# Kernel tuning notes

Hardware: AMD Instinct MI355X
Metric: run time of the kernel (lower is better)

The kernel has to match this reference:

```python
import jax, jax.numpy as jnp
import numpy as np

N, E, C, ED = 50000, 800000, 128, 16
NEG_SLOPE = 0.2


def setup_inputs() -> dict:
    key = jax.random.key(0)
    ks = jax.random.split(key, 18)
    inp = {
        "h": jax.random.normal(ks[0], (N, C), jnp.float32),
        "edge_index": jax.random.randint(ks[1], (2, E), 0, N),
        "edge_attr": jax.random.normal(ks[2], (E, ED), jnp.float32),
        "reducible": jax.random.randint(ks[3], (N,), 0, 2) > 0,
    }
    names = ["W", "att_src", "att_dst", "W_edge", "att_edge", "W_res", "bias"]
    shapes = [(C, C), (C,), (C,), (ED, C), (C,), (C, C), (C,)]
    i = 4
    for pre in ["red_", "irr_"]:
        for n, sh in zip(names, shapes):
            inp[pre + n] = jax.random.normal(ks[i], sh, jnp.float32) * 0.05
            i += 1
    return inp


def _gat_conv(h, src, dst, edge_attr, W, att_src, att_dst, W_edge, att_edge, W_res, bias):
    """PyG GATConv (heads=1, residual=True, add_self_loops=True, fill_value='mean')."""
    n = h.shape[0]
    # self-loop edge_attr = mean of incoming edge_attr per node (0 if none)
    sum_attr = jax.ops.segment_sum(edge_attr, dst, num_segments=n)
    cnt = jax.ops.segment_sum(jnp.ones((edge_attr.shape[0],), edge_attr.dtype), dst, num_segments=n)
    mean_attr = sum_attr / jnp.maximum(cnt, 1.0)[:, None]
    loop = jnp.arange(n)
    s = jnp.concatenate([src, loop])   # [E+N]
    d = jnp.concatenate([dst, loop])   # [E+N]
    ea = jnp.concatenate([edge_attr, mean_attr], axis=0)  # [E+N, ED]
    x = h @ W                              # [N, C]
    a_src = x @ att_src                    # [N]
    a_dst = x @ att_dst                    # [N]
    a_edge = (ea @ W_edge) @ att_edge      # [E+N]
    alpha = jax.nn.leaky_relu(a_src[s] + a_dst[d] + a_edge, NEG_SLOPE)
    # per-destination softmax (every node has a self-loop -> denom > 0)
    m = jax.ops.segment_max(alpha, d, num_segments=n)
    ex = jnp.exp(alpha - m[d])
    denom = jax.ops.segment_sum(ex, d, num_segments=n)
    w = ex / denom[d]                      # [E+N]
    out = jax.ops.segment_sum(w[:, None] * x[s], d, num_segments=n)  # [N, C]
    return out + h @ W_res + bias


def reference(h, edge_index, edge_attr, reducible,
              red_W, red_att_src, red_att_dst, red_W_edge, red_att_edge, red_W_res, red_bias,
              irr_W, irr_att_src, irr_att_dst, irr_W_edge, irr_att_edge, irr_W_res, irr_bias):
    src, dst = edge_index[0], edge_index[1]
    out_r = _gat_conv(h, src, dst, edge_attr, red_W, red_att_src, red_att_dst,
                      red_W_edge, red_att_edge, red_W_res, red_bias)
    out_i = _gat_conv(h, src, dst, edge_attr, irr_W, irr_att_src, irr_att_dst,
                      irr_W_edge, irr_att_edge, irr_W_res, irr_bias)
    return jax.nn.relu(jnp.where(reducible[:, None], out_r, out_i))
```

## Files before the change

### kernel.cpp

```cpp
#include <hip/hip_runtime.h>
#include <hip/hip_bf16.h>

#define CDIM 128
#define EDIM 16
#define NEG_SLOPE 0.2f

typedef __attribute__((ext_vector_type(8))) short bf16x8;
typedef __attribute__((ext_vector_type(4))) float f32x4;
typedef __attribute__((ext_vector_type(2))) float f32x2;
typedef unsigned int uint;
typedef unsigned short ushort;

__device__ __forceinline__ ushort f2bf(float f) {
    uint u = __float_as_uint(f);
    return (ushort)((u + 0x7fffu + ((u >> 16) & 1u)) >> 16);
}
__device__ __forceinline__ uint packbf(float lo, float hi) {
    return ((uint)f2bf(hi) << 16) | (uint)f2bf(lo);
}
__device__ __forceinline__ float bflo(uint w) { return __uint_as_float(w << 16); }
__device__ __forceinline__ float bfhi(uint w) { return __uint_as_float(w & 0xffff0000u); }

__device__ __forceinline__ bool redtest(const void* red, int i, int notInt, int notFloat) {
    if (!notInt)        return ((const int*)red)[i] != 0;
    else if (!notFloat) return ((const float*)red)[i] != 0.f;
    else                return ((const unsigned char*)red)[i] != 0;
}

__global__ void bcatwe_kernel(const float* __restrict__ Wr, const float* __restrict__ Wi,
                              const float* __restrict__ Wrr, const float* __restrict__ Wri,
                              ushort* __restrict__ BT,
                              const float* __restrict__ WeR, const float* __restrict__ aeR,
                              const float* __restrict__ WeI, const float* __restrict__ aeI,
                              float* __restrict__ we) {
    if (blockIdx.x < 256) {
        int idx = blockIdx.x * 256 + threadIdx.x;
        int c = idx >> 7, k = idx & 127;
        const float* srcm;
        if (c < 128)      srcm = Wr;
        else if (c < 256) srcm = Wi;
        else if (c < 384) srcm = Wrr;
        else              srcm = Wri;
        BT[idx] = f2bf(srcm[k * 128 + (c & 127)]);
    } else {
        int lane = threadIdx.x;
        if (lane < 16) {
            float s = 0.f;
            for (int c = 0; c < CDIM; ++c) s += WeR[lane * CDIM + c] * aeR[c];
            we[lane] = s;
        } else if (lane < 32) {
            int j = lane - 16;
            float s = 0.f;
            for (int c = 0; c < CDIM; ++c) s += WeI[j * CDIM + c] * aeI[c];
            we[16 + j] = s;
        }
    }
}

__global__ __launch_bounds__(256) void prep_kernel(const uint* __restrict__ red, int nwords,
                                                   int* __restrict__ flags,
                                                   const int* __restrict__ dst, int* __restrict__ cnt,
                                                   int* __restrict__ rank,
                                                   const float* __restrict__ ea, const float* __restrict__ we,
                                                   uint* __restrict__ escal4,
                                                   const float* __restrict__ h, ushort* __restrict__ hbf,
                                                   int E, int n4) {
    int i = blockIdx.x * 256 + threadIdx.x;
    if (i < nwords) {
        uint w = red[i];
        bool isInt = (w <= 1u);
        bool isFloat = (w == 0u) || (w == 0x3f800000u);
        if (!isInt) atomicOr(&flags[0], 1);
        if (!isFloat) atomicOr(&flags[1], 1);
    }
    if (i < E) {
        int r = atomicAdd(&cnt[dst[i]], 1);
        __builtin_nontemporal_store(r, rank + i);
        const f32x4* row = (const f32x4*)(ea + (size_t)i * EDIM);
        const float4* we4 = (const float4*)we;
        float er = 0.f, ei = 0.f;
#pragma unroll
        for (int q = 0; q < 4; ++q) {
            f32x4 v = __builtin_nontemporal_load(row + q);
            float4 wr = we4[q], wi = we4[4 + q];
            er += v.x * wr.x + v.y * wr.y + v.z * wr.z + v.w * wr.w;
            ei += v.x * wi.x + v.y * wi.y + v.z * wi.z + v.w * wi.w;
        }
        __builtin_nontemporal_store(packbf(er, ei), escal4 + i);
    }
    if (i < n4) {
        f32x4 v = __builtin_nontemporal_load((const f32x4*)h + i);
        uint2 o;
        o.x = packbf(v.x, v.y);
        o.y = packbf(v.z, v.w);
        ((uint2*)hbf)[i] = o;
    }
}

__global__ __launch_bounds__(256) void gemm_dots(const ushort* __restrict__ A,
                                                 const ushort* __restrict__ BT,
                                                 ushort* __restrict__ C,
                                                 const float* __restrict__ attsr, const float* __restrict__ attdr,
                                                 const float* __restrict__ attsi, const float* __restrict__ attdi,
                                                 float* __restrict__ asr, float* __restrict__ adr,
                                                 float* __restrict__ asi, float* __restrict__ adi,
                                                 int M) {
    __shared__ ushort As[128 * 128];
    __shared__ ushort Bs[128 * 128];
    __shared__ float dots[4][128];
    int t = threadIdx.x;
    int lane = t & 63, wv = t >> 6;
    int rb = blockIdx.x * 128;

    if (t < 128) { dots[0][t] = 0.f; dots[1][t] = 0.f; dots[2][t] = 0.f; dots[3][t] = 0.f; }

    int rsub = wv * 4 + (lane >> 4);
    int c0 = lane & 15;
#pragma unroll
    for (int p = 0; p < 8; ++p) {
        int row = p * 16 + rsub;
        int chunk = c0 ^ (row & 7);
        int gra = rb + row; if (gra > M - 1) gra = M - 1;
        const ushort* ga = A + (size_t)gra * 128 + chunk * 8;
        __builtin_amdgcn_global_load_lds(
            (const __attribute__((address_space(1))) void*)ga,
            (__attribute__((address_space(3))) void*)((char*)As + p * 4096 + wv * 1024),
            16, 0, 0);
    }

    int wr = wv >> 1, wc = wv & 1;
    int l15 = lane & 15, l4 = lane >> 4;
    const char* Ab = (const char*)As;
    const char* Bb = (const char*)Bs;

    for (int s = 0; s < 4; ++s) {
#pragma unroll
        for (int p = 0; p < 8; ++p) {
            int row = p * 16 + rsub;
            int chunk = c0 ^ (row & 7);
            const ushort* gb = BT + (size_t)(s * 128 + row) * 128 + chunk * 8;
            __builtin_amdgcn_global_load_lds(
                (const __attribute__((address_space(1))) void*)gb,
                (__attribute__((address_space(3))) void*)((char*)Bs + p * 4096 + wv * 1024),
                16, 0, 0);
        }
        __syncthreads();

        f32x4 acc[4][4];
#pragma unroll
        for (int i = 0; i < 4; ++i)
#pragma unroll
            for (int j = 0; j < 4; ++j) acc[i][j] = (f32x4){0.f, 0.f, 0.f, 0.f};

#pragma unroll
        for (int ks = 0; ks < 4; ++ks) {
            bf16x8 a[4], b[4];
#pragma unroll
            for (int f = 0; f < 4; ++f) {
                int row = wr * 64 + f * 16 + l15;
                int ch = (ks * 4 + l4) ^ (row & 7);
                a[f] = *(const bf16x8*)(Ab + row * 256 + ch * 16);
                int col = wc * 64 + f * 16 + l15;
                int ch2 = (ks * 4 + l4) ^ (col & 7);
                b[f] = *(const bf16x8*)(Bb + col * 256 + ch2 * 16);
            }
#pragma unroll
            for (int i = 0; i < 4; ++i)
#pragma unroll
                for (int j = 0; j < 4; ++j)
                    acc[i][j] = __builtin_amdgcn_mfma_f32_16x16x32_bf16(a[i], b[j], acc[i][j], 0, 0, 0);
        }

        if (s < 2) {
            const float* attS = s ? attsi : attsr;
            const float* attD = s ? attdi : attdr;
            float aS[4], aD[4];
#pragma unroll
            for (int j = 0; j < 4; ++j) {
                int c = wc * 64 + j * 16 + l15;
                aS[j] = attS[c]; aD[j] = attD[c];
            }
#pragma unroll
            for (int i = 0; i < 4; ++i)
#pragma unroll
                for (int rr = 0; rr < 4; ++rr) {
                    float ps = 0.f, pd = 0.f;
#pragma unroll
                    for (int j = 0; j < 4; ++j) {
                        float v = acc[i][j][rr];
                        ps += v * aS[j]; pd += v * aD[j];
                    }
#pragma unroll
                    for (int d = 1; d < 16; d <<= 1) {
                        ps += __shfl_xor(ps, d); pd += __shfl_xor(pd, d);
                    }
                    if (l15 == 0) {
                        int row = wr * 64 + i * 16 + l4 * 4 + rr;
                        atomicAdd(&dots[s * 2 + 0][row], ps);
                        atomicAdd(&dots[s * 2 + 1][row], pd);
                    }
                }
        }

#pragma unroll
        for (int i = 0; i < 4; ++i) {
            int rl = wr * 64 + i * 16 + l4 * 4;
#pragma unroll
            for (int j = 0; j < 4; ++j) {
                int col = s * 128 + wc * 64 + j * 16 + l15;
#pragma unroll
                for (int r = 0; r < 4; ++r) {
                    int gr = rb + rl + r;
                    if (gr < M) C[(size_t)gr * 512 + col] = f2bf(acc[i][j][r]);
                }
            }
        }
        __syncthreads();
    }

    if (t < 128) {
        int gr = rb + t;
        if (gr < M) {
            asr[gr] = dots[0][t]; adr[gr] = dots[1][t];
            asi[gr] = dots[2][t]; adi[gr] = dots[3][t];
        }
    }
}

__global__ __launch_bounds__(256) void scanA_kernel(const int* __restrict__ cnt,
                                                    int* __restrict__ offA,
                                                    int* __restrict__ bsum, int n) {
    __shared__ int wsum[4];
    int t = threadIdx.x, lane = t & 63, wid = t >> 6;
    int i0 = blockIdx.x * 1024 + t * 4;
    int v[4];
#pragma unroll
    for (int j = 0; j < 4; ++j) { int i = i0 + j; v[j] = (i < n) ? cnt[i] : 0; }
    int s = v[0] + v[1] + v[2] + v[3];
    int incl = s;
#pragma unroll
    for (int d = 1; d < 64; d <<= 1) { int u = __shfl_up(incl, d); if (lane >= d) incl += u; }
    if (lane == 63) wsum[wid] = incl;
    __syncthreads();
    int wpre = 0;
    for (int w = 0; w < wid; ++w) wpre += wsum[w];
    int run = wpre + incl - s;
#pragma unroll
    for (int j = 0; j < 4; ++j) {
        int i = i0 + j;
        if (i < n) offA[i] = run;
        run += v[j];
    }
    if (t == 255) bsum[blockIdx.x] = wpre + incl;
}

__global__ void scanB_kernel(int* __restrict__ bsum, int nb) {
    int lane = threadIdx.x;
    int carry = 0;
    for (int base = 0; base < nb; base += 64) {
        int i = base + lane;
        int v = (i < nb) ? bsum[i] : 0;
        int incl = v;
#pragma unroll
        for (int d = 1; d < 64; d <<= 1) { int u = __shfl_up(incl, d); if (lane >= d) incl += u; }
        if (i < nb) bsum[i] = carry + incl - v;
        carry += __shfl(incl, 63);
    }
}

__global__ __launch_bounds__(256) void scatter_kernel(
    const int* __restrict__ src, const int* __restrict__ dst,
    const int* __restrict__ rank, const uint* __restrict__ escal4,
    const void* __restrict__ red, const int* __restrict__ flags,
    const int* __restrict__ offA, const int* __restrict__ bsum,
    uint* __restrict__ csr, int E) {
    int e = blockIdx.x * 256 + threadIdx.x;
    if (e >= E) return;
    int s = __builtin_nontemporal_load(src + e);
    int d = __builtin_nontemporal_load(dst + e);
    uint ee = __builtin_nontemporal_load(escal4 + e);
    int rk = __builtin_nontemporal_load(rank + e);
    int notInt = flags[0], notFloat = flags[1];
    bool rr = redtest(red, d, notInt, notFloat);
    uint evb = rr ? (ee & 0xffffu) : (ee >> 16);
    int off = offA[d] + bsum[d >> 10];
    csr[off + rk] = (uint)s | (evb << 16);
}

__global__ __launch_bounds__(256) void node_kernel(
    const ushort* __restrict__ xcat,
    const float* __restrict__ adst_r, const float* __restrict__ adst_i,
    const float* __restrict__ asrc_r, const float* __restrict__ asrc_i,
    const void* __restrict__ red, const int* __restrict__ flags,
    const int* __restrict__ offA, const int* __restrict__ bsum,
    const uint* __restrict__ csr,
    const float* __restrict__ bias_r, const float* __restrict__ bias_i,
    float* __restrict__ out, int n, int E) {
    __shared__ uint2 buf[4][64];
    int wv = threadIdx.x >> 6, lane = threadIdx.x & 63;
    int node = blockIdx.x * 4 + wv;
    if (node >= n) return;

    int notInt = flags[0], notFloat = flags[1];
    bool r = redtest(red, node, notInt, notFloat);

    const float* asrc = r ? asrc_r : asrc_i;
    float adst = (r ? adst_r : adst_i)[node];
    uint vsel = r ? 0u : 256u;
    int b0 = offA[node] + bsum[node >> 10];
    int b1 = (node + 1 < n) ? (offA[node + 1] + bsum[(node + 1) >> 10]) : E;
    int k = b1 - b0;
    const char* xb = (const char*)xcat;
    uint lane4 = lane * 4;

    float m = -1e30f, denom = 0.f;
    float2 acca = make_float2(0.f, 0.f), accb = make_float2(0.f, 0.f);
    float sumE = 0.f;

    for (int base = b0; base < b1; base += 64) {
        int j = base + lane;
        float al = -1e30f; uint soff = 0;
        if (j < b1) {
            uint rec = __builtin_nontemporal_load(csr + j);
            uint s = rec & 0xffffu;
            float ev = bfhi(rec);
            sumE += ev;
            soff = s * 1024u + vsel;
            float a = asrc[s] + ev + adst;
            al = (a >= 0.f) ? a : NEG_SLOPE * a;
        }
        float cm = al;
#pragma unroll
        for (int d = 32; d; d >>= 1) cm = fmaxf(cm, __shfl_xor(cm, d));
        float mn = fmaxf(m, cm);
        float sc = __expf(m - mn);
        denom *= sc;
        acca.x *= sc; acca.y *= sc; accb.x *= sc; accb.y *= sc;
        m = mn;
        float ex = (j < b1) ? __expf(al - mn) : 0.f;
        buf[wv][lane] = make_uint2(__float_as_uint(ex), soff);
        __builtin_amdgcn_wave_barrier();
        int cc = min(64, b1 - base);
        int ccp = (cc + 7) & ~7;
        for (int tq = 0; tq < ccp; tq += 8) {
            uint2 u[8];
#pragma unroll
            for (int q = 0; q < 8; ++q) u[q] = buf[wv][tq + q];
            uint v[8];
#pragma unroll
            for (int q = 0; q < 8; ++q) v[q] = *(const uint*)(xb + u[q].y + lane4);
#pragma unroll
            for (int q = 0; q < 4; ++q) {
                float w = __uint_as_float(u[q].x);
                acca.x += w * bflo(v[q]); acca.y += w * bfhi(v[q]);
            }
#pragma unroll
            for (int q = 4; q < 8; ++q) {
                float w = __uint_as_float(u[q].x);
                accb.x += w * bflo(v[q]); accb.y += w * bfhi(v[q]);
            }
        }
        float exs = ex;
#pragma unroll
        for (int d = 32; d; d >>= 1) exs += __shfl_xor(exs, d);
        denom += exs;
        __builtin_amdgcn_wave_barrier();
    }
    float acc0 = acca.x + accb.x, acc1 = acca.y + accb.y;

#pragma unroll
    for (int d = 32; d; d >>= 1) sumE += __shfl_xor(sumE, d);
    float eself = sumE / fmaxf((float)k, 1.f);
    float a = asrc[node] + adst + eself;
    float aself = (a >= 0.f) ? a : NEG_SLOPE * a;
    float mn = fmaxf(m, aself);
    float sc = __expf(m - mn);
    float exl = __expf(aself - mn);
    denom = denom * sc + exl;
    uint voff = (uint)node * 1024u + vsel;
    uint vsw = *(const uint*)(xb + voff + lane4);
    acc0 = acc0 * sc + exl * bflo(vsw);
    acc1 = acc1 * sc + exl * bfhi(vsw);

    float inv = 1.f / denom;
    uint roff = (uint)node * 1024u + (r ? 512u : 768u);
    uint bw = *(const uint*)(xb + roff + lane4);
    float2 bi2 = ((const float2*)(r ? bias_r : bias_i))[lane];
    f32x2 o;
    o.x = fmaxf(acc0 * inv + bflo(bw) + bi2.x, 0.f);
    o.y = fmaxf(acc1 * inv + bfhi(bw) + bi2.y, 0.f);
    __builtin_nontemporal_store(o, ((f32x2*)out) + (size_t)node * 64 + lane);
}

extern "C" void kernel_launch(void* const* d_in, const int* in_sizes, int n_in,
                              void* d_out, int out_size, void* d_ws, size_t ws_size,
                              hipStream_t stream) {
    const float* h          = (const float*)d_in[0];
    const int*   edge_index = (const int*)d_in[1];
    const float* edge_attr  = (const float*)d_in[2];
    const void*  reducible  = d_in[3];
    const float* red_W      = (const float*)d_in[4];
    const float* red_att_src= (const float*)d_in[5];
    const float* red_att_dst= (const float*)d_in[6];
    const float* red_W_edge = (const float*)d_in[7];
    const float* red_att_edge=(const float*)d_in[8];
    const float* red_W_res  = (const float*)d_in[9];
    const float* red_bias   = (const float*)d_in[10];
    const float* irr_W      = (const float*)d_in[11];
    const float* irr_att_src= (const float*)d_in[12];
    const float* irr_att_dst= (const float*)d_in[13];
    const float* irr_W_edge = (const float*)d_in[14];
    const float* irr_att_edge=(const float*)d_in[15];
    const float* irr_W_res  = (const float*)d_in[16];
    const float* irr_bias   = (const float*)d_in[17];

    const int N = in_sizes[0] / CDIM;
    const int E = in_sizes[1] / 2;
    const int* src = edge_index;
    const int* dst = edge_index + E;
    const int nb = (N + 1023) / 1024;
    const int n4 = N * 128 / 4;

    float* out = (float*)d_out;

    size_t cur = 0;
    auto alloc = [&](size_t bytes) { size_t p = cur; cur = (cur + bytes + 255) & ~(size_t)255; return p; };
    char* ws = (char*)d_ws;
    size_t o_xcat  = alloc((size_t)N * 512 * 2);
    size_t o_hbf   = alloc((size_t)N * 128 * 2);
    size_t o_bcat  = alloc(512 * 128 * 2);
    size_t o_we    = alloc(256);
    size_t o_asr   = alloc((size_t)N * 4);
    size_t o_adr   = alloc((size_t)N * 4);
    size_t o_asi   = alloc((size_t)N * 4);
    size_t o_adi   = alloc((size_t)N * 4);
    size_t o_flags = alloc(256);
    size_t o_cnt   = alloc((size_t)N * 4);
    size_t o_offA  = alloc((size_t)N * 4);
    size_t o_bsum  = alloc((size_t)(nb + 1) * 4);
    size_t o_rank  = alloc((size_t)E * 4);
    size_t o_escal = alloc((size_t)E * 4);
    size_t o_csr   = alloc((size_t)E * 4);
    if (cur > ws_size) return;

    ushort* xcat = (ushort*)(ws + o_xcat);
    ushort* hbf  = (ushort*)(ws + o_hbf);
    ushort* bcat = (ushort*)(ws + o_bcat);
    float* we    = (float*)(ws + o_we);
    float* asr   = (float*)(ws + o_asr);
    float* adr   = (float*)(ws + o_adr);
    float* asi   = (float*)(ws + o_asi);
    float* adi   = (float*)(ws + o_adi);
    int*   flags = (int*)(ws + o_flags);
    int*   cnt   = (int*)(ws + o_cnt);
    int*   offA  = (int*)(ws + o_offA);
    int*   bsum  = (int*)(ws + o_bsum);
    int*   rank  = (int*)(ws + o_rank);
    uint*  escal4= (uint*)(ws + o_escal);
    uint*  csr   = (uint*)(ws + o_csr);

    hipMemsetAsync(flags, 0, 8, stream);
    hipMemsetAsync(cnt, 0, (size_t)N * 4, stream);

    bcatwe_kernel<<<257, 256, 0, stream>>>(red_W, irr_W, red_W_res, irr_W_res, bcat,
                                           red_W_edge, red_att_edge, irr_W_edge, irr_att_edge, we);

    int nwords = N / 4;
    int pgrid = (max(E, n4) + 255) / 256;
    prep_kernel<<<pgrid, 256, 0, stream>>>((const uint*)reducible, nwords, flags,
                                           dst, cnt, rank, edge_attr, we, escal4,
                                           h, hbf, E, n4);

    gemm_dots<<<(N + 127) / 128, 256, 0, stream>>>(hbf, bcat, xcat,
                                                   red_att_src, red_att_dst,
                                                   irr_att_src, irr_att_dst,
                                                   asr, adr, asi, adi, N);

    scanA_kernel<<<nb, 256, 0, stream>>>(cnt, offA, bsum, N);
    scanB_kernel<<<1, 64, 0, stream>>>(bsum, nb);

    scatter_kernel<<<(E + 255) / 256, 256, 0, stream>>>(src, dst, rank, escal4,
                                                        reducible, flags, offA, bsum, csr, E);

    node_kernel<<<(N + 3) / 4, 256, 0, stream>>>(xcat, adr, adi, asr, asi,
                                                 reducible, flags, offA, bsum, csr,
                                                 red_bias, irr_bias, out, N, E);
}
```

Baseline: 152.8 us.

## Split degree counters into 8 slices and drop online-max softmax in node kernel

The per-destination atomic counters used to build the CSR are split into 8 copies, chosen by block index, to reduce atomic contention. The slice id is packed into the rank's high bits, and scanA turns the slices into per-slice prefix offsets that scatter then adds. Separately, node_kernel drops the running-max softmax (wave max reductions and rescaling) and uses exp clamped at 60 with a single final sum reduction. This removes per-chunk shuffles, but it assumes the logits stay small enough to avoid overflow or precision loss. The counter memset and the scanA reads grow eightfold.

```diff
diff --git a/kernel.cpp b/kernel.cpp
--- a/kernel.cpp
+++ b/kernel.cpp
@@ -59,13 +59,14 @@
 
 __global__ __launch_bounds__(256) void prep_kernel(const uint* __restrict__ red, int nwords,
                                                    int* __restrict__ flags,
-                                                   const int* __restrict__ dst, int* __restrict__ cnt,
+                                                   const int* __restrict__ dst, int* __restrict__ cnt8,
                                                    int* __restrict__ rank,
                                                    const float* __restrict__ ea, const float* __restrict__ we,
                                                    uint* __restrict__ escal4,
                                                    const float* __restrict__ h, ushort* __restrict__ hbf,
-                                                   int E, int n4) {
+                                                   int N, int E, int n4) {
     int i = blockIdx.x * 256 + threadIdx.x;
+    int c = blockIdx.x & 7;
     if (i < nwords) {
         uint w = red[i];
         bool isInt = (w <= 1u);
@@ -74,8 +75,9 @@
         if (!isFloat) atomicOr(&flags[1], 1);
     }
     if (i < E) {
-        int r = atomicAdd(&cnt[dst[i]], 1);
-        __builtin_nontemporal_store(r, rank + i);
+        int d = dst[i];
+        int rk = atomicAdd(&cnt8[c * N + d], 1);
+        __builtin_nontemporal_store(rk | (c << 28), rank + i);
         const f32x4* row = (const f32x4*)(ea + (size_t)i * EDIM);
         const float4* we4 = (const float4*)we;
         float er = 0.f, ei = 0.f;
@@ -227,7 +229,7 @@
     }
 }
 
-__global__ __launch_bounds__(256) void scanA_kernel(const int* __restrict__ cnt,
+__global__ __launch_bounds__(256) void scanA_kernel(int* __restrict__ cnt8,
                                                     int* __restrict__ offA,
                                                     int* __restrict__ bsum, int n) {
     __shared__ int wsum[4];
@@ -235,7 +237,19 @@
     int i0 = blockIdx.x * 1024 + t * 4;
     int v[4];
 #pragma unroll
-    for (int j = 0; j < 4; ++j) { int i = i0 + j; v[j] = (i < n) ? cnt[i] : 0; }
+    for (int j = 0; j < 4; ++j) {
+        int d = i0 + j;
+        int tot = 0;
+        if (d < n) {
+#pragma unroll
+            for (int x = 0; x < 8; ++x) {
+                int cv = cnt8[x * n + d];
+                cnt8[x * n + d] = tot;
+                tot += cv;
+            }
+        }
+        v[j] = tot;
+    }
     int s = v[0] + v[1] + v[2] + v[3];
     int incl = s;
 #pragma unroll
@@ -273,17 +287,20 @@
     const int* __restrict__ rank, const uint* __restrict__ escal4,
     const void* __restrict__ red, const int* __restrict__ flags,
     const int* __restrict__ offA, const int* __restrict__ bsum,
-    uint* __restrict__ csr, int E) {
+    const int* __restrict__ cnt8,
+    uint* __restrict__ csr, int N, int E) {
     int e = blockIdx.x * 256 + threadIdx.x;
     if (e >= E) return;
     int s = __builtin_nontemporal_load(src + e);
     int d = __builtin_nontemporal_load(dst + e);
     uint ee = __builtin_nontemporal_load(escal4 + e);
-    int rk = __builtin_nontemporal_load(rank + e);
+    int rkw = __builtin_nontemporal_load(rank + e);
+    int c = ((uint)rkw) >> 28;
+    int rk = rkw & 0x0fffffff;
     int notInt = flags[0], notFloat = flags[1];
     bool rr = redtest(red, d, notInt, notFloat);
     uint evb = rr ? (ee & 0xffffu) : (ee >> 16);
-    int off = offA[d] + bsum[d >> 10];
+    int off = offA[d] + bsum[d >> 10] + cnt8[c * N + d];
     csr[off + rk] = (uint)s | (evb << 16);
 }
 
@@ -313,13 +330,12 @@
     const char* xb = (const char*)xcat;
     uint lane4 = lane * 4;
 
-    float m = -1e30f, denom = 0.f;
+    float denom_l = 0.f, sumE = 0.f;
     float2 acca = make_float2(0.f, 0.f), accb = make_float2(0.f, 0.f);
-    float sumE = 0.f;
 
     for (int base = b0; base < b1; base += 64) {
         int j = base + lane;
-        float al = -1e30f; uint soff = 0;
+        float ex = 0.f; uint soff = 0;
         if (j < b1) {
             uint rec = __builtin_nontemporal_load(csr + j);
             uint s = rec & 0xffffu;
@@ -327,17 +343,10 @@
             sumE += ev;
             soff = s * 1024u + vsel;
             float a = asrc[s] + ev + adst;
-            al = (a >= 0.f) ? a : NEG_SLOPE * a;
-        }
-        float cm = al;
-#pragma unroll
-        for (int d = 32; d; d >>= 1) cm = fmaxf(cm, __shfl_xor(cm, d));
-        float mn = fmaxf(m, cm);
-        float sc = __expf(m - mn);
-        denom *= sc;
-        acca.x *= sc; acca.y *= sc; accb.x *= sc; accb.y *= sc;
-        m = mn;
-        float ex = (j < b1) ? __expf(al - mn) : 0.f;
+            float al = (a >= 0.f) ? a : NEG_SLOPE * a;
+            ex = __expf(fminf(al, 60.f));
+            denom_l += ex;
+        }
         buf[wv][lane] = make_uint2(__float_as_uint(ex), soff);
         __builtin_amdgcn_wave_barrier();
         int cc = min(64, b1 - base);
@@ -360,27 +369,25 @@
                 accb.x += w * bflo(v[q]); accb.y += w * bfhi(v[q]);
             }
         }
-        float exs = ex;
-#pragma unroll
-        for (int d = 32; d; d >>= 1) exs += __shfl_xor(exs, d);
-        denom += exs;
         __builtin_amdgcn_wave_barrier();
     }
     float acc0 = acca.x + accb.x, acc1 = acca.y + accb.y;
 
 #pragma unroll
-    for (int d = 32; d; d >>= 1) sumE += __shfl_xor(sumE, d);
+    for (int d = 32; d; d >>= 1) {
+        sumE += __shfl_xor(sumE, d);
+        denom_l += __shfl_xor(denom_l, d);
+    }
+
     float eself = sumE / fmaxf((float)k, 1.f);
     float a = asrc[node] + adst + eself;
     float aself = (a >= 0.f) ? a : NEG_SLOPE * a;
-    float mn = fmaxf(m, aself);
-    float sc = __expf(m - mn);
-    float exl = __expf(aself - mn);
-    denom = denom * sc + exl;
+    float exl = __expf(fminf(aself, 60.f));
+    float denom = denom_l + exl;
     uint voff = (uint)node * 1024u + vsel;
     uint vsw = *(const uint*)(xb + voff + lane4);
-    acc0 = acc0 * sc + exl * bflo(vsw);
-    acc1 = acc1 * sc + exl * bfhi(vsw);
+    acc0 += exl * bflo(vsw);
+    acc1 += exl * bfhi(vsw);
 
     float inv = 1.f / denom;
     uint roff = (uint)node * 1024u + (r ? 512u : 768u);
@@ -435,7 +442,7 @@
     size_t o_asi   = alloc((size_t)N * 4);
     size_t o_adi   = alloc((size_t)N * 4);
     size_t o_flags = alloc(256);
-    size_t o_cnt   = alloc((size_t)N * 4);
+    size_t o_cnt8  = alloc((size_t)N * 8 * 4);
     size_t o_offA  = alloc((size_t)N * 4);
     size_t o_bsum  = alloc((size_t)(nb + 1) * 4);
     size_t o_rank  = alloc((size_t)E * 4);
@@ -452,7 +459,7 @@
     float* asi   = (float*)(ws + o_asi);
     float* adi   = (float*)(ws + o_adi);
     int*   flags = (int*)(ws + o_flags);
-    int*   cnt   = (int*)(ws + o_cnt);
+    int*   cnt8  = (int*)(ws + o_cnt8);
     int*   offA  = (int*)(ws + o_offA);
     int*   bsum  = (int*)(ws + o_bsum);
     int*   rank  = (int*)(ws + o_rank);
@@ -460,7 +467,7 @@
     uint*  csr   = (uint*)(ws + o_csr);
 
     hipMemsetAsync(flags, 0, 8, stream);
-    hipMemsetAsync(cnt, 0, (size_t)N * 4, stream);
+    hipMemsetAsync(cnt8, 0, (size_t)N * 8 * 4, stream);
 
     bcatwe_kernel<<<257, 256, 0, stream>>>(red_W, irr_W, red_W_res, irr_W_res, bcat,
                                            red_W_edge, red_att_edge, irr_W_edge, irr_att_edge, we);
@@ -468,19 +475,20 @@
     int nwords = N / 4;
     int pgrid = (max(E, n4) + 255) / 256;
     prep_kernel<<<pgrid, 256, 0, stream>>>((const uint*)reducible, nwords, flags,
-                                           dst, cnt, rank, edge_attr, we, escal4,
-                                           h, hbf, E, n4);
+                                           dst, cnt8, rank, edge_attr, we, escal4,
+                                           h, hbf, N, E, n4);
 
     gemm_dots<<<(N + 127) / 128, 256, 0, stream>>>(hbf, bcat, xcat,
                                                    red_att_src, red_att_dst,
                                                    irr_att_src, irr_att_dst,
                                                    asr, adr, asi, adi, N);
 
-    scanA_kernel<<<nb, 256, 0, stream>>>(cnt, offA, bsum, N);
+    scanA_kernel<<<nb, 256, 0, stream>>>(cnt8, offA, bsum, N);
     scanB_kernel<<<1, 64, 0, stream>>>(bsum, nb);
 
     scatter_kernel<<<(E + 255) / 256, 256, 0, stream>>>(src, dst, rank, escal4,
-                                                        reducible, flags, offA, bsum, csr, E);
+                                                        reducible, flags, offA, bsum, cnt8,
+                                                        csr, N, E);
 
     node_kernel<<<(N + 3) / 4, 256, 0, stream>>>(xcat, adr, adi, asr, asi,
                                                  reducible, flags, offA, bsum, csr,
```

After: 152.4 us. No clear change (-0.2%).
